# Optimization experiments

Measured on AMD Instinct MI355X. Metric: run time of the kernel, lower is better.

The kernel has to match this reference:

```python
import jax, jax.numpy as jnp
import numpy as np

B_SZ, L, H, P, G, N, CS = 2, 2048, 32, 64, 1, 128, 256


def _i8(k, shape):
    return jax.random.randint(k, shape, -127, 128, dtype=jnp.int32).astype(jnp.int8)


def setup_inputs() -> dict:
    key = jax.random.key(0)
    k = jax.random.split(key, 7)
    return {
        "x": _i8(k[0], (B_SZ, L, H, P)),          # quantized int8 activations
        "dt": _i8(k[1], (B_SZ, L, H)),
        "B": _i8(k[2], (B_SZ, L, G, N)),
        "C": _i8(k[3], (B_SZ, L, G, N)),
        "q_A_log": _i8(k[4], (H,)),               # int8 quantized A_log
        "q_D": _i8(k[5], (H,)),                   # int8 quantized D (D_has_hdim=False)
        "dt_bias": jax.random.normal(k[6], (H,), jnp.float32) * 0.1,
        "A_log_scale": jnp.float32(0.02),
        "D_scale": jnp.float32(0.01),
        "dt_scale": jnp.float32(0.03),
        "x_scale": jnp.float32(0.05),
        "B_scale": jnp.float32(0.05),
        "C_scale": jnp.float32(0.05),
    }


def _chunk_scan(x, dt, B, C, q_A_log, q_D, dt_bias,
                A_log_scale, D_scale, dt_scale, x_scale, B_scale, C_scale):
    f32 = jnp.float32
    b, l, h, p = x.shape
    g, n = B.shape[2], B.shape[3]
    cs = CS
    nc = l // cs

    # --- inline dequantization (per-tensor scales, nhead/ndim groups == 0) ---
    xf = x.astype(f32) * x_scale                       # (b, l, h, p)
    dtf = jax.nn.softplus(dt.astype(f32) * dt_scale + dt_bias)   # (b, l, h), dt_limit=(0, inf)
    A = -jnp.exp(q_A_log.astype(f32) * A_log_scale)    # (h,)
    Bf = B.astype(f32) * B_scale                       # (b, l, g, n)
    Cf = C.astype(f32) * C_scale

    # --- chunk the sequence ---
    xc = xf.reshape(b, nc, cs, h, p)
    dtc = dtf.reshape(b, nc, cs, h)
    Bc = Bf.reshape(b, nc, cs, g, n)
    Cc = Cf.reshape(b, nc, cs, g, n)
    rep = h // g
    Bh = jnp.repeat(Bc, rep, axis=3)                   # (b, nc, cs, h, n)
    Ch = jnp.repeat(Cc, rep, axis=3)

    dA = dtc * A                                       # (b, nc, cs, h), <= 0
    cum = jnp.cumsum(dA, axis=2)                       # cumulative log-decay within chunk

    # --- per-chunk states: sum_s exp(cum[-1]-cum[s]) * dt[s] * B[s] (x) x[s] ---
    decay_states = jnp.exp(cum[:, :, -1:, :] - cum)    # (b, nc, cs, h)
    states = jnp.einsum('bzlhn,bzlh,bzlhp->bzhpn', Bh, dtc * decay_states, xc)

    # --- inter-chunk recurrence (sequential scan over chunks) ---
    chunk_decay = jnp.exp(cum[:, :, -1, :])            # (b, nc, h)

    def step(carry, inp):
        s_c, d_c = inp                                 # (b, h, p, n), (b, h)
        new = d_c[:, :, None, None] * carry + s_c
        return new, carry                              # emit state entering this chunk

    states_t = jnp.moveaxis(states, 1, 0)              # (nc, b, h, p, n)
    decay_t = jnp.moveaxis(chunk_decay, 1, 0)          # (nc, b, h)
    final_state, prev_states = jax.lax.scan(
        step, jnp.zeros((b, h, p, n), f32), (states_t, decay_t))
    prev_states = jnp.moveaxis(prev_states, 0, 1)      # (b, nc, h, p, n)

    # --- inter-chunk output: C[l] . state_in * exp(cum[l]) ---
    y_inter = jnp.einsum('bzlhn,bzhpn,bzlh->bzlhp', Ch, prev_states, jnp.exp(cum))

    # --- intra-chunk output: causal (C.B) attention with decay weights ---
    cumT = jnp.moveaxis(cum, 3, 2)                     # (b, nc, h, cs)
    diff = cumT[..., :, None] - cumT[..., None, :]     # (b, nc, h, cs, cs): cum[l]-cum[s]
    mask = jnp.tril(jnp.ones((cs, cs), bool))
    decay_m = jnp.exp(jnp.where(mask, diff, -jnp.inf)) # zero above diagonal, no overflow
    scores = (jnp.einsum('bzlhn,bzshn->bzhls', Ch, Bh)
              * decay_m
              * jnp.moveaxis(dtc, 3, 2)[..., None, :])
    y_intra = jnp.einsum('bzhls,bzshp->bzlhp', scores, xc)

    # --- skip connection D * x (per-head D) ---
    Df = q_D.astype(f32) * D_scale                     # (h,)
    y = (y_intra + y_inter).reshape(b, l, h, p) + xf * Df[None, None, :, None]
    return y


def reference(x, dt, B, C, q_A_log, q_D, dt_bias,
              A_log_scale, D_scale, dt_scale, x_scale, B_scale, C_scale):
    return _chunk_scan(x, dt, B, C, q_A_log, q_D, dt_bias,
                       A_log_scale, D_scale, dt_scale, x_scale, B_scale, C_scale)
```

## Files before the change

### kernel.cpp

```cpp
#include <hip/hip_runtime.h>
#include <math.h>

#define BB 2
#define LSEQ 2048
#define H 32
#define PDIM 64
#define NDIM 128
#define CS 256
#define NC 8

typedef _Float16 half8 __attribute__((ext_vector_type(8)));
typedef _Float16 half4 __attribute__((ext_vector_type(4)));
typedef float floatx4 __attribute__((ext_vector_type(4)));


__device__ __forceinline__ int dot4i8(int a, int b, int c) {
#if __has_builtin(__builtin_amdgcn_sdot4)
    return __builtin_amdgcn_sdot4(a, b, c, false);
#else
    c += ((a << 24) >> 24) * ((b << 24) >> 24);
    c += ((a << 16) >> 24) * ((b << 16) >> 24);
    c += ((a << 8) >> 24) * ((b << 8) >> 24);
    c += (a >> 24) * (b >> 24);
    return c;
#endif
}

__global__ __launch_bounds__(256) void kA(
    const int* __restrict__ Bm, const int* __restrict__ Cm,
    const float* __restrict__ Bs_p, const float* __restrict__ Cs_p,
    float* __restrict__ CBt, _Float16* __restrict__ Bt16T, _Float16* __restrict__ C16T)
{
    __shared__ int Bi[64][33];
    __shared__ int Ci[64][33];
    int t = threadIdx.x;
    int r = blockIdx.x % 26;
    int zz = blockIdx.x / 26;
    int z = zz & 7, b = zz >> 3;
    int bz = b * NC + z;
    if (r < 10) {
        const int LT[10] = {0,1,1,2,2,2,3,3,3,3};
        const int ST[10] = {0,0,1,0,1,2,0,1,2,3};
        int l0 = LT[r] * 64, s0 = ST[r] * 64;
        const int* Bp = Bm + (size_t)(b * LSEQ + z * CS + s0) * NDIM;
        const int* Cp = Cm + (size_t)(b * LSEQ + z * CS + l0) * NDIM;
        for (int i = t; i < 64 * 32; i += 256) {
            int rr = i >> 5, k = i & 31;
            const int* sb = Bp + rr * NDIM + k * 4;
            const int* sc = Cp + rr * NDIM + k * 4;
            Bi[rr][k] = (sb[0] & 255) | ((sb[1] & 255) << 8) | ((sb[2] & 255) << 16) | ((sb[3] & 255) << 24);
            Ci[rr][k] = (sc[0] & 255) | ((sc[1] & 255) << 8) | ((sc[2] & 255) << 16) | ((sc[3] & 255) << 24);
        }
        __syncthreads();
        float cbscale = (*Bs_p) * (*Cs_p);
        int ll = t & 63, lg = t >> 6;
        int acc[16];
#pragma unroll
        for (int i = 0; i < 16; ++i) acc[i] = 0;
        for (int k = 0; k < 32; ++k) {
            int cw = Ci[ll][k];
#pragma unroll
            for (int si = 0; si < 16; ++si)
                acc[si] = dot4i8(cw, Bi[lg * 16 + si][k], acc[si]);
        }
        int l = l0 + ll;
        int l16 = l >> 4, lm = l & 15;
        int sb8 = (s0 + lg * 16) >> 3;
        float* bp = CBt + ((size_t)(bz * 16 + l16) * 32 + sb8) * 128 + lm * 8;
#pragma unroll
        for (int g = 0; g < 2; ++g) {
            floatx4 v0, v1;
#pragma unroll
            for (int i = 0; i < 4; ++i) {
                v0[i] = (float)acc[g * 8 + i] * cbscale;
                v1[i] = (float)acc[g * 8 + 4 + i] * cbscale;
            }
            *(floatx4*)(bp + g * 128) = v0;
            *(floatx4*)(bp + g * 128 + 4) = v1;
        }
    } else {
        int slice = r - 10;
        {
            int lm = t >> 4, n8 = t & 15;
            const int* cp = Cm + (size_t)(b * LSEQ + z * CS + slice * 16 + lm) * NDIM + n8 * 8;
            int4 c0 = *(const int4*)cp;
            int4 c1 = *(const int4*)(cp + 4);
            half8 v;
            v[0] = (_Float16)(float)c0.x; v[1] = (_Float16)(float)c0.y;
            v[2] = (_Float16)(float)c0.z; v[3] = (_Float16)(float)c0.w;
            v[4] = (_Float16)(float)c1.x; v[5] = (_Float16)(float)c1.y;
            v[6] = (_Float16)(float)c1.z; v[7] = (_Float16)(float)c1.w;
            *(half8*)(C16T + ((size_t)(bz * 16 + slice) * 16 + n8) * 128 + lm * 8) = v;
        }
        {
            int nm = t & 15, s8l = t >> 4;
            int n16 = slice & 7, s8 = (slice >> 3) * 16 + s8l;
            const int* bp = Bm + (size_t)(b * LSEQ + z * CS + s8 * 8) * NDIM + n16 * 16 + nm;
            half8 v;
#pragma unroll
            for (int j = 0; j < 8; ++j) v[j] = (_Float16)(float)bp[(size_t)j * NDIM];
            *(half8*)(Bt16T + ((size_t)(bz * 8 + n16) * 32 + s8) * 128 + nm * 8) = v;
        }
    }
}

#define XC_PITCH 132
__global__ __launch_bounds__(256) void k013(
    const int* __restrict__ dt, const int* __restrict__ qA, const float* __restrict__ dt_bias,
    const float* __restrict__ A_scale_p, const float* __restrict__ dt_scale_p,
    const int* __restrict__ xq, const float* __restrict__ xs_p, const float* __restrict__ Bs_p,
    const _Float16* __restrict__ Bt16T,
    float* __restrict__ cum, float* __restrict__ cdecay,
    _Float16* __restrict__ xTdtT, signed char* __restrict__ x8,
    float* __restrict__ states)
{
    __shared__ float cumS[CS];
    __shared__ float cA[CS], cB[CS];
    __shared__ float wsum[4];
    __shared__ _Float16 xcS[4 * 32 * XC_PITCH];
    int t = threadIdx.x;
    int h = blockIdx.x & 31, z = (blockIdx.x >> 5) & 7, b = blockIdx.x >> 8;
    int bz = b * NC + z, bzh = bz * H + h;
    int lane6 = t & 63, w = t >> 6;

    float A = -__expf((float)qA[h] * (*A_scale_p));
    float raw = (float)dt[(size_t)(b * LSEQ + z * CS + t) * H + h];
    float xin = raw * (*dt_scale_p) + dt_bias[h];
    float sp = (xin > 20.f) ? xin : log1pf(__expf(xin));
    float v = sp * A;
#pragma unroll
    for (int off = 1; off < 64; off <<= 1) {
        float u = __shfl_up(v, off, 64);
        if (lane6 >= off) v += u;
    }
    if (lane6 == 63) wsum[w] = v;
    __syncthreads();
    float add = 0.f;
    for (int wv = 0; wv < w; ++wv) add += wsum[wv];
    float cumv = v + add;
    float cl = wsum[0] + wsum[1] + wsum[2] + wsum[3];
    float xs = *xs_p;
    cum[bzh * CS + t] = cumv;
    if (t == 0) cdecay[bzh] = __expf(cl);
    cumS[t] = cumv;
    cA[t] = sp * xs;
    cB[t] = sp * __expf(cl - cumv) * xs * (*Bs_p);
    __syncthreads();

    int s8 = t & 31, pg = t >> 5;
    const int* xb = xq + ((size_t)(b * LSEQ + z * CS) * H + h) * PDIM + pg * 8;
    {
        half8 va[8], vc[8];
        signed char pk[8][8];
#pragma unroll
        for (int j = 0; j < 8; ++j) {
            int s = s8 * 8 + j;
            const int* xp = xb + (size_t)s * (H * PDIM);
            int4 lo = *(const int4*)xp;
            int4 hi = *(const int4*)(xp + 4);
            float a = cA[s], c = cB[s];
#define CVT(PL, V) { float xv = (float)(V); va[PL][j] = (_Float16)(xv * a); vc[PL][j] = (_Float16)(xv * c); pk[j][PL] = (signed char)(V); }
            CVT(0, lo.x) CVT(1, lo.y) CVT(2, lo.z) CVT(3, lo.w)
            CVT(4, hi.x) CVT(5, hi.y) CVT(6, hi.z) CVT(7, hi.w)
#undef CVT
        }
        int p16 = pg >> 1;
#pragma unroll
        for (int pl = 0; pl < 8; ++pl) {
            int p = pg * 8 + pl;
            *(half8*)(xTdtT + ((size_t)(bzh * 4 + p16) * 32 + s8) * 128 + (p & 15) * 8) = va[pl];
            xcS[(p16 * 32 + s8) * XC_PITCH + (p & 15) * 8 + 0] = vc[pl][0];
        }
#pragma unroll
        for (int pl = 0; pl < 8; ++pl) {
            int p = pg * 8 + pl;
            *(half8*)(xcS + (p16 * 32 + s8) * XC_PITCH + (p & 15) * 8) = vc[pl];
        }
        signed char* x8b = x8 + ((size_t)(b * LSEQ + z * CS) * H + h) * PDIM + pg * 8;
#pragma unroll
        for (int j = 0; j < 8; ++j)
            *(int2*)(x8b + (size_t)(s8 * 8 + j) * (H * PDIM)) = *(int2*)pk[j];
    }
    __syncthreads();

    int m = lane6 & 15, q = lane6 >> 4;
    const _Float16* bbase = Bt16T + (size_t)(bz * 8) * 32 * 128 + m * 8;
    const _Float16* abase = xcS + (w * 32) * XC_PITCH + m * 8;
    floatx4 acc[8] = {};
    for (int kk = 0; kk < 8; ++kk) {
        if (cl - cumS[kk * 32 + 31] < -30.f) continue;
        int s8k = kk * 4 + q;
        half8 a = *(const half8*)(abase + s8k * XC_PITCH);
#pragma unroll
        for (int nt = 0; nt < 8; ++nt) {
            half8 bf = *(const half8*)(bbase + ((size_t)nt * 32 + s8k) * 128);
            acc[nt] = __builtin_amdgcn_mfma_f32_16x16x32_f16(a, bf, acc[nt], 0, 0, 0);
        }
    }
    float* sb = states + (size_t)bzh * (PDIM * NDIM);
#pragma unroll
    for (int nt = 0; nt < 8; ++nt)
#pragma unroll
        for (int rr = 0; rr < 4; ++rr)
            sb[(size_t)(w * 16 + q * 4 + rr) * NDIM + nt * 16 + m] = acc[nt][rr];
}

__global__ __launch_bounds__(256) void k4_scan(
    const float* __restrict__ cdecay, const float* __restrict__ states,
    _Float16* __restrict__ statesHT)
{
    int idx = blockIdx.x * 256 + threadIdx.x;
    int n4 = (idx & 31) * 4, p = (idx >> 5) & 63, h = (idx >> 11) & 31, b = idx >> 16;
    int soff = p * 128 + n4;
    int toff = ((p >> 4) * 16 + (n4 >> 3)) * 128 + (p & 15) * 8 + (n4 & 7);
    floatx4 carry = {};
    for (int z = 0; z < NC; ++z) {
        int bzh = (b * NC + z) * H + h;
        floatx4 v = *(const floatx4*)(states + (size_t)bzh * 8192 + soff);
        float d = cdecay[bzh];
        half4 o;
#pragma unroll
        for (int i = 0; i < 4; ++i) o[i] = (_Float16)(carry[i] * 0.0625f);
        *(half4*)(statesHT + (size_t)bzh * 8192 + toff) = o;
#pragma unroll
        for (int i = 0; i < 4; ++i) carry[i] = d * carry[i] + v[i];
    }
}

__global__ __launch_bounds__(256) void k56(
    const signed char* __restrict__ x8, const int* __restrict__ qD,
    const float* __restrict__ cum, const float* __restrict__ CBt,
    const _Float16* __restrict__ xTdtT, const _Float16* __restrict__ C16T,
    const _Float16* __restrict__ statesHT,
    const float* __restrict__ Cs_p, const float* __restrict__ xs_p, const float* __restrict__ Ds_p,
    float* __restrict__ out)
{
    __shared__ float cumL[CS];
    __shared__ float ep[128][65];
    int t = threadIdx.x;
    int h = blockIdx.x & 31, z = (blockIdx.x >> 5) & 7, b = blockIdx.x >> 8;
    int bz = b * NC + z, bzh = bz * H + h;
    cumL[t] = cum[bzh * CS + t];
    __syncthreads();
    int w = t >> 6, lane = t & 63, m = lane & 15, q = lane >> 4;
    floatx4 acc[4][4] = {};

    const _Float16* shb = statesHT + (size_t)bzh * 8192 + m * 8;
    const _Float16* cbase = C16T + (size_t)bz * 16 * 16 * 128 + m * 8;
    bool interact[4];
#pragma unroll
    for (int j = 0; j < 4; ++j) interact[j] = (cumL[(4 * j + w) * 16] > -80.f);
    for (int kk = 0; kk < 4; ++kk) {
        int n8 = kk * 4 + q;
        half8 bf[4];
#pragma unroll
        for (int pt = 0; pt < 4; ++pt)
            bf[pt] = *(const half8*)(shb + (pt * 16 + n8) * 128);
#pragma unroll
        for (int j = 0; j < 4; ++j) {
            if (!interact[j]) continue;
            half8 ha = *(const half8*)(cbase + ((size_t)(4 * j + w) * 16 + n8) * 128);
#pragma unroll
            for (int pt = 0; pt < 4; ++pt)
                acc[j][pt] = __builtin_amdgcn_mfma_f32_16x16x32_f16(ha, bf[pt], acc[j][pt], 0, 0, 0);
        }
    }
    float Cs16 = (*Cs_p) * 16.0f;
#pragma unroll
    for (int j = 0; j < 4; ++j)
#pragma unroll
        for (int r = 0; r < 4; ++r) {
            float e = __expf(cumL[(4 * j + w) * 16 + q * 4 + r]) * Cs16;
#pragma unroll
            for (int pt = 0; pt < 4; ++pt) acc[j][pt][r] *= e;
        }

    const float* cbtb = CBt + (size_t)bz * 16 * 32 * 128 + m * 8;
    const _Float16* xb = xTdtT + (size_t)bzh * 4 * 32 * 128 + m * 8;
    for (int kk = 0; kk < 8; ++kk) {
        int jmin = (2 * kk - w + 3) >> 2;
        if (jmin < 0) jmin = 0;
        if (jmin > 3) continue;
        int s8 = kk * 4 + q;
        half8 bf[4];
#pragma unroll
        for (int pt = 0; pt < 4; ++pt)
            bf[pt] = *(const half8*)(xb + ((size_t)pt * 32 + s8) * 128);
        float cs_hi = cumL[kk * 32 + 31];
#pragma unroll
        for (int j = 0; j < 4; ++j) {
            if (j < jmin) continue;
            int l16 = 4 * j + w;
            if (cumL[l16 * 16] - cs_hi < -30.f) continue;
            int lA = l16 * 16 + m;
            float cum_l = cumL[lA];
            const float* cp = cbtb + ((size_t)l16 * 32 + s8) * 128;
            floatx4 c0 = *(const floatx4*)cp;
            floatx4 c1 = *(const floatx4*)(cp + 4);
            half8 a;
#pragma unroll
            for (int jj = 0; jj < 8; ++jj) {
                int s = kk * 32 + q * 8 + jj;
                float cb = (jj < 4) ? c0[jj] : c1[jj - 4];
                float wv = cb * __expf(cum_l - cumL[s]);
                a[jj] = (_Float16)((s <= lA) ? wv : 0.f);
            }
#pragma unroll
            for (int pt = 0; pt < 4; ++pt)
                acc[j][pt] = __builtin_amdgcn_mfma_f32_16x16x32_f16(a, bf[pt], acc[j][pt], 0, 0, 0);
        }
    }

    float xsDf = (*xs_p) * ((float)qD[h] * (*Ds_p));
    __syncthreads();
#pragma unroll
    for (int pass = 0; pass < 2; ++pass) {
#pragma unroll
        for (int jj = 0; jj < 2; ++jj) {
            int j = pass * 2 + jj;
            int lbase = (((4 * j + w) * 16) & 127) + q * 4;
#pragma unroll
            for (int r = 0; r < 4; ++r)
#pragma unroll
                for (int pt = 0; pt < 4; ++pt)
                    ep[lbase + r][pt * 16 + m] = acc[j][pt][r];
        }
        __syncthreads();
        int lloc = t >> 1;
        int l = pass * 128 + lloc;
        size_t go = ((size_t)(b * LSEQ + z * CS + l) * H + h) * PDIM + (t & 1) * 32;
        const float* er = &ep[lloc][(t & 1) * 32];
        const signed char* xp8 = x8 + go;
#pragma unroll
        for (int it = 0; it < 8; ++it) {
            int xw = *(const int*)(xp8 + it * 4);
            floatx4 v;
            v[0] = er[it * 4 + 0] + (float)((xw << 24) >> 24) * xsDf;
            v[1] = er[it * 4 + 1] + (float)((xw << 16) >> 24) * xsDf;
            v[2] = er[it * 4 + 2] + (float)((xw << 8) >> 24) * xsDf;
            v[3] = er[it * 4 + 3] + (float)(xw >> 24) * xsDf;
            *(floatx4*)(out + go + it * 4) = v;
        }
        __syncthreads();
    }
}

extern "C" void kernel_launch(void* const* d_in, const int* in_sizes, int n_in,
                              void* d_out, int out_size, void* d_ws, size_t ws_size,
                              hipStream_t stream)
{
    const int* xq = (const int*)d_in[0];
    const int* dt = (const int*)d_in[1];
    const int* Bm = (const int*)d_in[2];
    const int* Cm = (const int*)d_in[3];
    const int* qA = (const int*)d_in[4];
    const int* qD = (const int*)d_in[5];
    const float* dt_bias = (const float*)d_in[6];
    const float* A_scale = (const float*)d_in[7];
    const float* D_scale = (const float*)d_in[8];
    const float* dt_scale = (const float*)d_in[9];
    const float* x_scale = (const float*)d_in[10];
    const float* B_scale = (const float*)d_in[11];
    const float* C_scale = (const float*)d_in[12];
    float* out = (float*)d_out;

    char* ws = (char*)d_ws;
    float* cum          = (float*)(ws);
    float* cdecay       = (float*)(ws + 524288);
    float* CBt          = (float*)(ws + 526336);
    float* states       = (float*)(ws + 4720640);
    _Float16* xTdtT     = (_Float16*)(ws + 21497856);
    _Float16* statesHT  = (_Float16*)(ws + 38275072);
    _Float16* Bt16T     = (_Float16*)(ws + 46663680);
    _Float16* C16T      = (_Float16*)(ws + 47712256);
    signed char* x8     = (signed char*)(ws + 48760832);

    kA<<<dim3(416), dim3(256), 0, stream>>>(Bm, Cm, B_scale, C_scale, CBt, Bt16T, C16T);
    k013<<<dim3(512), dim3(256), 0, stream>>>(dt, qA, dt_bias, A_scale, dt_scale,
                                              xq, x_scale, B_scale, Bt16T,
                                              cum, cdecay, xTdtT, x8, states);
    k4_scan<<<dim3(512), dim3(256), 0, stream>>>(cdecay, states, statesHT);
    k56<<<dim3(512), dim3(256), 0, stream>>>(x8, qD, cum, CBt, xTdtT, C16T, statesHT,
                                             C_scale, x_scale, D_scale, out);
}
```

Before: 163.5 us.

## Split k013 and k56 work across twice as many blocks with balanced row pairing

New measurement: 169.3 us. +3.5%, slower.

```diff
diff --git a/kernel.cpp b/kernel.cpp
--- a/kernel.cpp
+++ b/kernel.cpp
@@ -117,9 +117,10 @@
     __shared__ float cumS[CS];
     __shared__ float cA[CS], cB[CS];
     __shared__ float wsum[4];
-    __shared__ _Float16 xcS[4 * 32 * XC_PITCH];
+    __shared__ _Float16 xcS[2 * 32 * XC_PITCH];
     int t = threadIdx.x;
-    int h = blockIdx.x & 31, z = (blockIdx.x >> 5) & 7, b = blockIdx.x >> 8;
+    int half = blockIdx.x & 1;
+    int h = (blockIdx.x >> 1) & 31, z = (blockIdx.x >> 6) & 7, b = blockIdx.x >> 9;
     int bz = b * NC + z, bzh = bz * H + h;
     int lane6 = t & 63, w = t >> 6;
 
@@ -140,69 +141,64 @@
     float cumv = v + add;
     float cl = wsum[0] + wsum[1] + wsum[2] + wsum[3];
     float xs = *xs_p;
-    cum[bzh * CS + t] = cumv;
-    if (t == 0) cdecay[bzh] = __expf(cl);
+    if (half == 0) {
+        cum[bzh * CS + t] = cumv;
+        if (t == 0) cdecay[bzh] = __expf(cl);
+    }
     cumS[t] = cumv;
     cA[t] = sp * xs;
     cB[t] = sp * __expf(cl - cumv) * xs * (*Bs_p);
     __syncthreads();
 
-    int s8 = t & 31, pg = t >> 5;
-    const int* xb = xq + ((size_t)(b * LSEQ + z * CS) * H + h) * PDIM + pg * 8;
+    int s8 = t & 31, pq = t >> 5;
+    const int* xb = xq + ((size_t)(b * LSEQ + z * CS) * H + h) * PDIM + half * 32 + pq * 4;
+    signed char* x8b = x8 + ((size_t)(b * LSEQ + z * CS) * H + h) * PDIM + half * 32 + pq * 4;
     {
-        half8 va[8], vc[8];
-        signed char pk[8][8];
+        half8 va[4], vc[4];
 #pragma unroll
         for (int j = 0; j < 8; ++j) {
             int s = s8 * 8 + j;
-            const int* xp = xb + (size_t)s * (H * PDIM);
-            int4 lo = *(const int4*)xp;
-            int4 hi = *(const int4*)(xp + 4);
+            int4 w4 = *(const int4*)(xb + (size_t)s * (H * PDIM));
             float a = cA[s], c = cB[s];
-#define CVT(PL, V) { float xv = (float)(V); va[PL][j] = (_Float16)(xv * a); vc[PL][j] = (_Float16)(xv * c); pk[j][PL] = (signed char)(V); }
-            CVT(0, lo.x) CVT(1, lo.y) CVT(2, lo.z) CVT(3, lo.w)
-            CVT(4, hi.x) CVT(5, hi.y) CVT(6, hi.z) CVT(7, hi.w)
+            signed char pk[4];
+#define CVT(PL, V) { float xv = (float)(V); va[PL][j] = (_Float16)(xv * a); vc[PL][j] = (_Float16)(xv * c); pk[PL] = (signed char)(V); }
+            CVT(0, w4.x) CVT(1, w4.y) CVT(2, w4.z) CVT(3, w4.w)
 #undef CVT
-        }
-        int p16 = pg >> 1;
-#pragma unroll
-        for (int pl = 0; pl < 8; ++pl) {
-            int p = pg * 8 + pl;
-            *(half8*)(xTdtT + ((size_t)(bzh * 4 + p16) * 32 + s8) * 128 + (p & 15) * 8) = va[pl];
-            xcS[(p16 * 32 + s8) * XC_PITCH + (p & 15) * 8 + 0] = vc[pl][0];
-        }
-#pragma unroll
-        for (int pl = 0; pl < 8; ++pl) {
-            int p = pg * 8 + pl;
-            *(half8*)(xcS + (p16 * 32 + s8) * XC_PITCH + (p & 15) * 8) = vc[pl];
-        }
-        signed char* x8b = x8 + ((size_t)(b * LSEQ + z * CS) * H + h) * PDIM + pg * 8;
-#pragma unroll
-        for (int j = 0; j < 8; ++j)
-            *(int2*)(x8b + (size_t)(s8 * 8 + j) * (H * PDIM)) = *(int2*)pk[j];
+            *(int*)pk;
+            *(int*)(x8b + (size_t)s * (H * PDIM)) = *(int*)pk;
+        }
+#pragma unroll
+        for (int pl = 0; pl < 4; ++pl) {
+            int ploc = pq * 4 + pl;
+            int p16l = ploc >> 4, pm = ploc & 15;
+            *(half8*)(xTdtT + ((size_t)(bzh * 4 + half * 2 + p16l) * 32 + s8) * 128 + pm * 8) = va[pl];
+            *(half8*)(xcS + (p16l * 32 + s8) * XC_PITCH + pm * 8) = vc[pl];
+        }
     }
     __syncthreads();
 
     int m = lane6 & 15, q = lane6 >> 4;
-    const _Float16* bbase = Bt16T + (size_t)(bz * 8) * 32 * 128 + m * 8;
-    const _Float16* abase = xcS + (w * 32) * XC_PITCH + m * 8;
-    floatx4 acc[8] = {};
+    int p16l = w & 1, ntb = (w >> 1) * 4;
+    const _Float16* abase = xcS + (p16l * 32) * XC_PITCH + m * 8;
+    const _Float16* bbase = Bt16T + ((size_t)(bz * 8 + ntb) * 32) * 128 + m * 8;
+    floatx4 acc[4] = {};
     for (int kk = 0; kk < 8; ++kk) {
         if (cl - cumS[kk * 32 + 31] < -30.f) continue;
         int s8k = kk * 4 + q;
         half8 a = *(const half8*)(abase + s8k * XC_PITCH);
 #pragma unroll
-        for (int nt = 0; nt < 8; ++nt) {
-            half8 bf = *(const half8*)(bbase + ((size_t)nt * 32 + s8k) * 128);
-            acc[nt] = __builtin_amdgcn_mfma_f32_16x16x32_f16(a, bf, acc[nt], 0, 0, 0);
-        }
-    }
+        for (int i = 0; i < 4; ++i) {
+            half8 bf = *(const half8*)(bbase + ((size_t)i * 32 + s8k) * 128);
+            acc[i] = __builtin_amdgcn_mfma_f32_16x16x32_f16(a, bf, acc[i], 0, 0, 0);
+        }
+    }
+    int p16 = half * 2 + p16l;
     float* sb = states + (size_t)bzh * (PDIM * NDIM);
 #pragma unroll
-    for (int nt = 0; nt < 8; ++nt)
+    for (int i = 0; i < 4; ++i)
 #pragma unroll
         for (int rr = 0; rr < 4; ++rr)
-            sb[(size_t)(w * 16 + q * 4 + rr) * NDIM + nt * 16 + m] = acc[nt][rr];
+            sb[(size_t)(p16 * 16 + q * 4 + rr) * NDIM + (ntb + i) * 16 + m] = acc[i][rr];
 }
 
 __global__ __launch_bounds__(256) void k4_scan(
@@ -238,18 +234,20 @@
     __shared__ float cumL[CS];
     __shared__ float ep[128][65];
     int t = threadIdx.x;
-    int h = blockIdx.x & 31, z = (blockIdx.x >> 5) & 7, b = blockIdx.x >> 8;
+    int parity = blockIdx.x & 1;
+    int h = (blockIdx.x >> 1) & 31, z = (blockIdx.x >> 6) & 7, b = blockIdx.x >> 9;
     int bz = b * NC + z, bzh = bz * H + h;
     cumL[t] = cum[bzh * CS + t];
     __syncthreads();
     int w = t >> 6, lane = t & 63, m = lane & 15, q = lane >> 4;
-    floatx4 acc[4][4] = {};
+    int l16a[2] = {parity + 2 * w, parity + 2 * (7 - w)};
+    floatx4 acc[2][4] = {};
 
     const _Float16* shb = statesHT + (size_t)bzh * 8192 + m * 8;
     const _Float16* cbase = C16T + (size_t)bz * 16 * 16 * 128 + m * 8;
-    bool interact[4];
-#pragma unroll
-    for (int j = 0; j < 4; ++j) interact[j] = (cumL[(4 * j + w) * 16] > -80.f);
+    bool interact[2];
+#pragma unroll
+    for (int j = 0; j < 2; ++j) interact[j] = (cumL[l16a[j] * 16] > -80.f);
     for (int kk = 0; kk < 4; ++kk) {
         int n8 = kk * 4 + q;
         half8 bf[4];
@@ -257,9 +255,9 @@
         for (int pt = 0; pt < 4; ++pt)
             bf[pt] = *(const half8*)(shb + (pt * 16 + n8) * 128);
 #pragma unroll
-        for (int j = 0; j < 4; ++j) {
+        for (int j = 0; j < 2; ++j) {
             if (!interact[j]) continue;
-            half8 ha = *(const half8*)(cbase + ((size_t)(4 * j + w) * 16 + n8) * 128);
+            half8 ha = *(const half8*)(cbase + ((size_t)l16a[j] * 16 + n8) * 128);
 #pragma unroll
             for (int pt = 0; pt < 4; ++pt)
                 acc[j][pt] = __builtin_amdgcn_mfma_f32_16x16x32_f16(ha, bf[pt], acc[j][pt], 0, 0, 0);
@@ -267,10 +265,10 @@
     }
     float Cs16 = (*Cs_p) * 16.0f;
 #pragma unroll
-    for (int j = 0; j < 4; ++j)
+    for (int j = 0; j < 2; ++j)
 #pragma unroll
         for (int r = 0; r < 4; ++r) {
-            float e = __expf(cumL[(4 * j + w) * 16 + q * 4 + r]) * Cs16;
+            float e = __expf(cumL[l16a[j] * 16 + q * 4 + r]) * Cs16;
 #pragma unroll
             for (int pt = 0; pt < 4; ++pt) acc[j][pt][r] *= e;
         }
@@ -278,20 +276,20 @@
     const float* cbtb = CBt + (size_t)bz * 16 * 32 * 128 + m * 8;
     const _Float16* xb = xTdtT + (size_t)bzh * 4 * 32 * 128 + m * 8;
     for (int kk = 0; kk < 8; ++kk) {
-        int jmin = (2 * kk - w + 3) >> 2;
-        if (jmin < 0) jmin = 0;
-        if (jmin > 3) continue;
+        bool ex[2];
+#pragma unroll
+        for (int j = 0; j < 2; ++j)
+            ex[j] = (2 * kk <= l16a[j]) && (cumL[l16a[j] * 16] - cumL[kk * 32 + 31] >= -30.f);
+        if (!ex[0] && !ex[1]) continue;
         int s8 = kk * 4 + q;
         half8 bf[4];
 #pragma unroll
         for (int pt = 0; pt < 4; ++pt)
             bf[pt] = *(const half8*)(xb + ((size_t)pt * 32 + s8) * 128);
-        float cs_hi = cumL[kk * 32 + 31];
-#pragma unroll
-        for (int j = 0; j < 4; ++j) {
-            if (j < jmin) continue;
-            int l16 = 4 * j + w;
-            if (cumL[l16 * 16] - cs_hi < -30.f) continue;
+#pragma unroll
+        for (int j = 0; j < 2; ++j) {
+            if (!ex[j]) continue;
+            int l16 = l16a[j];
             int lA = l16 * 16 + m;
             float cum_l = cumL[lA];
             const float* cp = cbtb + ((size_t)l16 * 32 + s8) * 128;
@@ -314,34 +312,31 @@
     float xsDf = (*xs_p) * ((float)qD[h] * (*Ds_p));
     __syncthreads();
 #pragma unroll
-    for (int pass = 0; pass < 2; ++pass) {
-#pragma unroll
-        for (int jj = 0; jj < 2; ++jj) {
-            int j = pass * 2 + jj;
-            int lbase = (((4 * j + w) * 16) & 127) + q * 4;
-#pragma unroll
-            for (int r = 0; r < 4; ++r)
-#pragma unroll
-                for (int pt = 0; pt < 4; ++pt)
-                    ep[lbase + r][pt * 16 + m] = acc[j][pt][r];
-        }
-        __syncthreads();
-        int lloc = t >> 1;
-        int l = pass * 128 + lloc;
-        size_t go = ((size_t)(b * LSEQ + z * CS + l) * H + h) * PDIM + (t & 1) * 32;
-        const float* er = &ep[lloc][(t & 1) * 32];
-        const signed char* xp8 = x8 + go;
-#pragma unroll
-        for (int it = 0; it < 8; ++it) {
-            int xw = *(const int*)(xp8 + it * 4);
-            floatx4 v;
-            v[0] = er[it * 4 + 0] + (float)((xw << 24) >> 24) * xsDf;
-            v[1] = er[it * 4 + 1] + (float)((xw << 16) >> 24) * xsDf;
-            v[2] = er[it * 4 + 2] + (float)((xw << 8) >> 24) * xsDf;
-            v[3] = er[it * 4 + 3] + (float)(xw >> 24) * xsDf;
-            *(floatx4*)(out + go + it * 4) = v;
-        }
-        __syncthreads();
+    for (int j = 0; j < 2; ++j) {
+        int kidx = (j == 0) ? w : 7 - w;
+        int lbase = kidx * 16 + q * 4;
+#pragma unroll
+        for (int r = 0; r < 4; ++r)
+#pragma unroll
+            for (int pt = 0; pt < 4; ++pt)
+                ep[lbase + r][pt * 16 + m] = acc[j][pt][r];
+    }
+    __syncthreads();
+    int lloc = t >> 1;
+    int kidx = lloc >> 4, row = lloc & 15;
+    int l = (parity + 2 * kidx) * 16 + row;
+    size_t go = ((size_t)(b * LSEQ + z * CS + l) * H + h) * PDIM + (t & 1) * 32;
+    const float* er = &ep[lloc][(t & 1) * 32];
+    const signed char* xp8 = x8 + go;
+#pragma unroll
+    for (int it = 0; it < 8; ++it) {
+        int xw = *(const int*)(xp8 + it * 4);
+        floatx4 vv;
+        vv[0] = er[it * 4 + 0] + (float)((xw << 24) >> 24) * xsDf;
+        vv[1] = er[it * 4 + 1] + (float)((xw << 16) >> 24) * xsDf;
+        vv[2] = er[it * 4 + 2] + (float)((xw << 8) >> 24) * xsDf;
+        vv[3] = er[it * 4 + 3] + (float)(xw >> 24) * xsDf;
+        *(floatx4*)(out + go + it * 4) = vv;
     }
 }
 
@@ -376,10 +371,10 @@
     signed char* x8     = (signed char*)(ws + 48760832);
 
     kA<<<dim3(416), dim3(256), 0, stream>>>(Bm, Cm, B_scale, C_scale, CBt, Bt16T, C16T);
-    k013<<<dim3(512), dim3(256), 0, stream>>>(dt, qA, dt_bias, A_scale, dt_scale,
-                                              xq, x_scale, B_scale, Bt16T,
-                                              cum, cdecay, xTdtT, x8, states);
+    k013<<<dim3(1024), dim3(256), 0, stream>>>(dt, qA, dt_bias, A_scale, dt_scale,
+                                               xq, x_scale, B_scale, Bt16T,
+                                               cum, cdecay, xTdtT, x8, states);
     k4_scan<<<dim3(512), dim3(256), 0, stream>>>(cdecay, states, statesHT);
-    k56<<<dim3(512), dim3(256), 0, stream>>>(x8, qD, cum, CBt, xTdtT, C16T, statesHT,
-                                             C_scale, x_scale, D_scale, out);
-}
+    k56<<<dim3(1024), dim3(256), 0, stream>>>(x8, qD, cum, CBt, xTdtT, C16T, statesHT,
+                                              C_scale, x_scale, D_scale, out);
+}
```

## Fuse chunk-state compute with inter-chunk scan and rebuild x*dt in output kernel

Applied to the files above, without the earlier changes.

Result: slower. 232.6 us (+42.2%).

```diff
diff --git a/kernel.cpp b/kernel.cpp
--- a/kernel.cpp
+++ b/kernel.cpp
@@ -10,7 +10,6 @@
 #define NC 8
 
 typedef _Float16 half8 __attribute__((ext_vector_type(8)));
-typedef _Float16 half4 __attribute__((ext_vector_type(4)));
 typedef float floatx4 __attribute__((ext_vector_type(4)));
 
 
@@ -29,7 +28,7 @@
 __global__ __launch_bounds__(256) void kA(
     const int* __restrict__ Bm, const int* __restrict__ Cm,
     const float* __restrict__ Bs_p, const float* __restrict__ Cs_p,
-    float* __restrict__ CBt, _Float16* __restrict__ Bt16T, _Float16* __restrict__ C16T)
+    _Float16* __restrict__ CBh, _Float16* __restrict__ Bt16T, _Float16* __restrict__ C16T)
 {
     __shared__ int Bi[64][33];
     __shared__ int Ci[64][33];
@@ -66,17 +65,13 @@
         int l = l0 + ll;
         int l16 = l >> 4, lm = l & 15;
         int sb8 = (s0 + lg * 16) >> 3;
-        float* bp = CBt + ((size_t)(bz * 16 + l16) * 32 + sb8) * 128 + lm * 8;
+        _Float16* bp = CBh + ((size_t)(bz * 16 + l16) * 32 + sb8) * 128 + lm * 8;
 #pragma unroll
         for (int g = 0; g < 2; ++g) {
-            floatx4 v0, v1;
-#pragma unroll
-            for (int i = 0; i < 4; ++i) {
-                v0[i] = (float)acc[g * 8 + i] * cbscale;
-                v1[i] = (float)acc[g * 8 + 4 + i] * cbscale;
-            }
-            *(floatx4*)(bp + g * 128) = v0;
-            *(floatx4*)(bp + g * 128 + 4) = v1;
+            half8 v;
+#pragma unroll
+            for (int i = 0; i < 8; ++i) v[i] = (_Float16)((float)acc[g * 8 + i] * cbscale);
+            *(half8*)(bp + g * 128) = v;
         }
     } else {
         int slice = r - 10;
@@ -104,144 +99,139 @@
     }
 }
 
-#define XC_PITCH 132
-__global__ __launch_bounds__(256) void k013(
+#define XCB_PITCH 264
+__global__ __launch_bounds__(256) void kB(
     const int* __restrict__ dt, const int* __restrict__ qA, const float* __restrict__ dt_bias,
     const float* __restrict__ A_scale_p, const float* __restrict__ dt_scale_p,
     const int* __restrict__ xq, const float* __restrict__ xs_p, const float* __restrict__ Bs_p,
     const _Float16* __restrict__ Bt16T,
-    float* __restrict__ cum, float* __restrict__ cdecay,
-    _Float16* __restrict__ xTdtT, signed char* __restrict__ x8,
-    float* __restrict__ states)
+    float* __restrict__ cum, float* __restrict__ cA,
+    signed char* __restrict__ x8, _Float16* __restrict__ statesHT)
 {
-    __shared__ float cumS[CS];
-    __shared__ float cA[CS], cB[CS];
+    __shared__ _Float16 xcS[16 * XCB_PITCH];
     __shared__ float wsum[4];
-    __shared__ _Float16 xcS[4 * 32 * XC_PITCH];
+    __shared__ float cumS8[8];
     int t = threadIdx.x;
-    int h = blockIdx.x & 31, z = (blockIdx.x >> 5) & 7, b = blockIdx.x >> 8;
-    int bz = b * NC + z, bzh = bz * H + h;
+    int h = blockIdx.x & 31, b = (blockIdx.x >> 5) & 1;
+    int pq = (blockIdx.x >> 6) & 3, nh = blockIdx.x >> 8;
     int lane6 = t & 63, w = t >> 6;
-
+    int m = lane6 & 15, q = lane6 >> 4;
+    int ntg = nh * 4 + w;
     float A = -__expf((float)qA[h] * (*A_scale_p));
-    float raw = (float)dt[(size_t)(b * LSEQ + z * CS + t) * H + h];
-    float xin = raw * (*dt_scale_p) + dt_bias[h];
-    float sp = (xin > 20.f) ? xin : log1pf(__expf(xin));
-    float v = sp * A;
-#pragma unroll
-    for (int off = 1; off < 64; off <<= 1) {
-        float u = __shfl_up(v, off, 64);
-        if (lane6 >= off) v += u;
-    }
-    if (lane6 == 63) wsum[w] = v;
-    __syncthreads();
-    float add = 0.f;
-    for (int wv = 0; wv < w; ++wv) add += wsum[wv];
-    float cumv = v + add;
-    float cl = wsum[0] + wsum[1] + wsum[2] + wsum[3];
-    float xs = *xs_p;
-    cum[bzh * CS + t] = cumv;
-    if (t == 0) cdecay[bzh] = __expf(cl);
-    cumS[t] = cumv;
-    cA[t] = sp * xs;
-    cB[t] = sp * __expf(cl - cumv) * xs * (*Bs_p);
-    __syncthreads();
-
-    int s8 = t & 31, pg = t >> 5;
-    const int* xb = xq + ((size_t)(b * LSEQ + z * CS) * H + h) * PDIM + pg * 8;
-    {
-        half8 va[8], vc[8];
-        signed char pk[8][8];
-#pragma unroll
-        for (int j = 0; j < 8; ++j) {
-            int s = s8 * 8 + j;
-            const int* xp = xb + (size_t)s * (H * PDIM);
-            int4 lo = *(const int4*)xp;
-            int4 hi = *(const int4*)(xp + 4);
-            float a = cA[s], c = cB[s];
-#define CVT(PL, V) { float xv = (float)(V); va[PL][j] = (_Float16)(xv * a); vc[PL][j] = (_Float16)(xv * c); pk[j][PL] = (signed char)(V); }
-            CVT(0, lo.x) CVT(1, lo.y) CVT(2, lo.z) CVT(3, lo.w)
-            CVT(4, hi.x) CVT(5, hi.y) CVT(6, hi.z) CVT(7, hi.w)
-#undef CVT
-        }
-        int p16 = pg >> 1;
-#pragma unroll
-        for (int pl = 0; pl < 8; ++pl) {
-            int p = pg * 8 + pl;
-            *(half8*)(xTdtT + ((size_t)(bzh * 4 + p16) * 32 + s8) * 128 + (p & 15) * 8) = va[pl];
-            xcS[(p16 * 32 + s8) * XC_PITCH + (p & 15) * 8 + 0] = vc[pl][0];
-        }
-#pragma unroll
-        for (int pl = 0; pl < 8; ++pl) {
-            int p = pg * 8 + pl;
-            *(half8*)(xcS + (p16 * 32 + s8) * XC_PITCH + (p & 15) * 8) = vc[pl];
-        }
-        signed char* x8b = x8 + ((size_t)(b * LSEQ + z * CS) * H + h) * PDIM + pg * 8;
-#pragma unroll
-        for (int j = 0; j < 8; ++j)
-            *(int2*)(x8b + (size_t)(s8 * 8 + j) * (H * PDIM)) = *(int2*)pk[j];
-    }
-    __syncthreads();
-
-    int m = lane6 & 15, q = lane6 >> 4;
-    const _Float16* bbase = Bt16T + (size_t)(bz * 8) * 32 * 128 + m * 8;
-    const _Float16* abase = xcS + (w * 32) * XC_PITCH + m * 8;
-    floatx4 acc[8] = {};
-    for (int kk = 0; kk < 8; ++kk) {
-        if (cl - cumS[kk * 32 + 31] < -30.f) continue;
-        int s8k = kk * 4 + q;
-        half8 a = *(const half8*)(abase + s8k * XC_PITCH);
-#pragma unroll
-        for (int nt = 0; nt < 8; ++nt) {
-            half8 bf = *(const half8*)(bbase + ((size_t)nt * 32 + s8k) * 128);
-            acc[nt] = __builtin_amdgcn_mfma_f32_16x16x32_f16(a, bf, acc[nt], 0, 0, 0);
-        }
-    }
-    float* sb = states + (size_t)bzh * (PDIM * NDIM);
-#pragma unroll
-    for (int nt = 0; nt < 8; ++nt)
-#pragma unroll
-        for (int rr = 0; rr < 4; ++rr)
-            sb[(size_t)(w * 16 + q * 4 + rr) * NDIM + nt * 16 + m] = acc[nt][rr];
-}
-
-__global__ __launch_bounds__(256) void k4_scan(
-    const float* __restrict__ cdecay, const float* __restrict__ states,
-    _Float16* __restrict__ statesHT)
-{
-    int idx = blockIdx.x * 256 + threadIdx.x;
-    int n4 = (idx & 31) * 4, p = (idx >> 5) & 63, h = (idx >> 11) & 31, b = idx >> 16;
-    int soff = p * 128 + n4;
-    int toff = ((p >> 4) * 16 + (n4 >> 3)) * 128 + (p & 15) * 8 + (n4 & 7);
-    floatx4 carry = {};
+    float dts = *dt_scale_p, bias = dt_bias[h];
+    float xs = *xs_p, Bs = *Bs_p;
+    bool wr_meta = (pq == 0 && nh == 0);
+    bool wr_x8 = (nh == 0);
+    float carry[4] = {0.f, 0.f, 0.f, 0.f};
+
+    float rawv = (float)dt[(size_t)(b * LSEQ + t) * H + h];
+    const int* xp0 = xq + ((size_t)(b * LSEQ + t) * H + h) * PDIM + pq * 16;
+    int4 xw0 = *(const int4*)xp0, xw1 = *(const int4*)(xp0 + 4);
+    int4 xw2 = *(const int4*)(xp0 + 8), xw3 = *(const int4*)(xp0 + 12);
+
     for (int z = 0; z < NC; ++z) {
-        int bzh = (b * NC + z) * H + h;
-        floatx4 v = *(const floatx4*)(states + (size_t)bzh * 8192 + soff);
-        float d = cdecay[bzh];
-        half4 o;
-#pragma unroll
-        for (int i = 0; i < 4; ++i) o[i] = (_Float16)(carry[i] * 0.0625f);
-        *(half4*)(statesHT + (size_t)bzh * 8192 + toff) = o;
-#pragma unroll
-        for (int i = 0; i < 4; ++i) carry[i] = d * carry[i] + v[i];
-    }
-}
-
-__global__ __launch_bounds__(256) void k56(
+        int bz = b * NC + z, bzh = bz * H + h;
+        __syncthreads();
+        float xin = rawv * dts + bias;
+        float sp = (xin > 20.f) ? xin : log1pf(__expf(xin));
+        float v = sp * A;
+#pragma unroll
+        for (int off = 1; off < 64; off <<= 1) {
+            float u = __shfl_up(v, off, 64);
+            if (lane6 >= off) v += u;
+        }
+        if (lane6 == 63) wsum[w] = v;
+        __syncthreads();
+        float add = 0.f;
+        for (int wv = 0; wv < w; ++wv) add += wsum[wv];
+        float cumv = v + add;
+        float cl = wsum[0] + wsum[1] + wsum[2] + wsum[3];
+        if ((t & 31) == 31) cumS8[t >> 5] = cumv;
+        if (wr_meta) {
+            cum[(size_t)bzh * CS + t] = cumv;
+            cA[(size_t)bzh * CS + t] = sp * xs;
+        }
+        float cBv = sp * __expf(cl - cumv) * xs * Bs;
+        int xi[16] = {xw0.x, xw0.y, xw0.z, xw0.w, xw1.x, xw1.y, xw1.z, xw1.w,
+                      xw2.x, xw2.y, xw2.z, xw2.w, xw3.x, xw3.y, xw3.z, xw3.w};
+        signed char pk[16];
+#pragma unroll
+        for (int pl = 0; pl < 16; ++pl) {
+            xcS[pl * XCB_PITCH + t] = (_Float16)((float)xi[pl] * cBv);
+            pk[pl] = (signed char)xi[pl];
+        }
+        if (wr_x8)
+            *(int4*)(x8 + ((size_t)(b * LSEQ + z * CS + t) * H + h) * PDIM + pq * 16) = *(int4*)pk;
+        if (z + 1 < NC) {
+            rawv = (float)dt[(size_t)(b * LSEQ + (z + 1) * CS + t) * H + h];
+            const int* xp = xq + ((size_t)(b * LSEQ + (z + 1) * CS + t) * H + h) * PDIM + pq * 16;
+            xw0 = *(const int4*)xp; xw1 = *(const int4*)(xp + 4);
+            xw2 = *(const int4*)(xp + 8); xw3 = *(const int4*)(xp + 12);
+        }
+        __syncthreads();
+        floatx4 accz = {};
+        const _Float16* ab = xcS + m * XCB_PITCH;
+        const _Float16* bb = Bt16T + ((size_t)(bz * 8 + ntg) * 32) * 128 + m * 8;
+        for (int kk = 0; kk < 8; ++kk) {
+            if (cl - cumS8[kk] < -30.f) continue;
+            half8 a = *(const half8*)(ab + kk * 32 + q * 8);
+            half8 bf = *(const half8*)(bb + (size_t)(kk * 4 + q) * 128);
+            accz = __builtin_amdgcn_mfma_f32_16x16x32_f16(a, bf, accz, 0, 0, 0);
+        }
+        float dz = __expf(cl);
+        size_t sbase = (size_t)bzh * 8192 + (size_t)(pq * 16 + ntg * 2 + (m >> 3)) * 128 + (m & 7);
+#pragma unroll
+        for (int rr = 0; rr < 4; ++rr) {
+            statesHT[sbase + (q * 4 + rr) * 8] = (_Float16)(carry[rr] * 0.0625f);
+            carry[rr] = dz * carry[rr] + accz[rr];
+        }
+    }
+}
+
+#define XT_PITCH 136
+__global__ __launch_bounds__(256) void kC(
     const signed char* __restrict__ x8, const int* __restrict__ qD,
-    const float* __restrict__ cum, const float* __restrict__ CBt,
-    const _Float16* __restrict__ xTdtT, const _Float16* __restrict__ C16T,
+    const float* __restrict__ cum, const float* __restrict__ cA,
+    const _Float16* __restrict__ CBh, const _Float16* __restrict__ C16T,
     const _Float16* __restrict__ statesHT,
     const float* __restrict__ Cs_p, const float* __restrict__ xs_p, const float* __restrict__ Ds_p,
     float* __restrict__ out)
 {
     __shared__ float cumL[CS];
-    __shared__ float ep[128][65];
+    __shared__ __align__(16) char smem[4 * 32 * XT_PITCH * 2];
+    _Float16* xT = (_Float16*)smem;
+    float (*ep)[65] = (float(*)[65])smem;
     int t = threadIdx.x;
     int h = blockIdx.x & 31, z = (blockIdx.x >> 5) & 7, b = blockIdx.x >> 8;
     int bz = b * NC + z, bzh = bz * H + h;
-    cumL[t] = cum[bzh * CS + t];
+    cumL[t] = cum[(size_t)bzh * CS + t];
+    float cav = cA[(size_t)bzh * CS + t];
+
+    {
+        const signed char* xrow = x8 + ((size_t)(b * LSEQ + z * CS + t) * H + h) * PDIM;
+        int s8 = t >> 3, sj = t & 7;
+        int rw[4] = {((const int4*)xrow)->x, 0, 0, 0};
+        int4 r4 = *(const int4*)xrow;
+        int4 r5 = *(const int4*)(xrow + 16);
+        int4 r6 = *(const int4*)(xrow + 32);
+        int4 r7 = *(const int4*)(xrow + 48);
+        int words[16] = {r4.x, r4.y, r4.z, r4.w, r5.x, r5.y, r5.z, r5.w,
+                         r6.x, r6.y, r6.z, r6.w, r7.x, r7.y, r7.z, r7.w};
+        (void)rw;
+#pragma unroll
+        for (int wi = 0; wi < 16; ++wi) {
+            int wv = words[wi];
+#pragma unroll
+            for (int bi = 0; bi < 4; ++bi) {
+                int p = wi * 4 + bi;
+                int val = (wv << (24 - 8 * bi)) >> 24;
+                xT[((p >> 4) * 32 + s8) * XT_PITCH + (p & 15) * 8 + sj] =
+                    (_Float16)((float)val * cav);
+            }
+        }
+    }
     __syncthreads();
+
     int w = t >> 6, lane = t & 63, m = lane & 15, q = lane >> 4;
     floatx4 acc[4][4] = {};
 
@@ -275,8 +265,7 @@
             for (int pt = 0; pt < 4; ++pt) acc[j][pt][r] *= e;
         }
 
-    const float* cbtb = CBt + (size_t)bz * 16 * 32 * 128 + m * 8;
-    const _Float16* xb = xTdtT + (size_t)bzh * 4 * 32 * 128 + m * 8;
+    const _Float16* cbtb = CBh + (size_t)bz * 16 * 32 * 128 + m * 8;
     for (int kk = 0; kk < 8; ++kk) {
         int jmin = (2 * kk - w + 3) >> 2;
         if (jmin < 0) jmin = 0;
@@ -285,24 +274,19 @@
         half8 bf[4];
 #pragma unroll
         for (int pt = 0; pt < 4; ++pt)
-            bf[pt] = *(const half8*)(xb + ((size_t)pt * 32 + s8) * 128);
-        float cs_hi = cumL[kk * 32 + 31];
-#pragma unroll
-        for (int j = 0; j < 4; ++j) {
-            if (j < jmin) continue;
+            bf[pt] = *(const half8*)(xT + (size_t)(pt * 32 + s8) * XT_PITCH + m * 8);
+#pragma unroll
+        for (int j = jmin; j < 4; ++j) {
             int l16 = 4 * j + w;
-            if (cumL[l16 * 16] - cs_hi < -30.f) continue;
+            if (cumL[l16 * 16] - cumL[kk * 32 + 31] < -30.f) continue;
             int lA = l16 * 16 + m;
             float cum_l = cumL[lA];
-            const float* cp = cbtb + ((size_t)l16 * 32 + s8) * 128;
-            floatx4 c0 = *(const floatx4*)cp;
-            floatx4 c1 = *(const floatx4*)(cp + 4);
+            half8 cb8 = *(const half8*)(cbtb + ((size_t)l16 * 32 + s8) * 128);
             half8 a;
 #pragma unroll
             for (int jj = 0; jj < 8; ++jj) {
                 int s = kk * 32 + q * 8 + jj;
-                float cb = (jj < 4) ? c0[jj] : c1[jj - 4];
-                float wv = cb * __expf(cum_l - cumL[s]);
+                float wv = (float)cb8[jj] * __expf(cum_l - cumL[s]);
                 a[jj] = (_Float16)((s <= lA) ? wv : 0.f);
             }
 #pragma unroll
@@ -334,12 +318,12 @@
 #pragma unroll
         for (int it = 0; it < 8; ++it) {
             int xw = *(const int*)(xp8 + it * 4);
-            floatx4 v;
-            v[0] = er[it * 4 + 0] + (float)((xw << 24) >> 24) * xsDf;
-            v[1] = er[it * 4 + 1] + (float)((xw << 16) >> 24) * xsDf;
-            v[2] = er[it * 4 + 2] + (float)((xw << 8) >> 24) * xsDf;
-            v[3] = er[it * 4 + 3] + (float)(xw >> 24) * xsDf;
-            *(floatx4*)(out + go + it * 4) = v;
+            floatx4 vv;
+            vv[0] = er[it * 4 + 0] + (float)((xw << 24) >> 24) * xsDf;
+            vv[1] = er[it * 4 + 1] + (float)((xw << 16) >> 24) * xsDf;
+            vv[2] = er[it * 4 + 2] + (float)((xw << 8) >> 24) * xsDf;
+            vv[3] = er[it * 4 + 3] + (float)(xw >> 24) * xsDf;
+            *(floatx4*)(out + go + it * 4) = vv;
         }
         __syncthreads();
     }
@@ -366,20 +350,17 @@
 
     char* ws = (char*)d_ws;
     float* cum          = (float*)(ws);
-    float* cdecay       = (float*)(ws + 524288);
-    float* CBt          = (float*)(ws + 526336);
-    float* states       = (float*)(ws + 4720640);
-    _Float16* xTdtT     = (_Float16*)(ws + 21497856);
-    _Float16* statesHT  = (_Float16*)(ws + 38275072);
-    _Float16* Bt16T     = (_Float16*)(ws + 46663680);
-    _Float16* C16T      = (_Float16*)(ws + 47712256);
-    signed char* x8     = (signed char*)(ws + 48760832);
-
-    kA<<<dim3(416), dim3(256), 0, stream>>>(Bm, Cm, B_scale, C_scale, CBt, Bt16T, C16T);
-    k013<<<dim3(512), dim3(256), 0, stream>>>(dt, qA, dt_bias, A_scale, dt_scale,
-                                              xq, x_scale, B_scale, Bt16T,
-                                              cum, cdecay, xTdtT, x8, states);
-    k4_scan<<<dim3(512), dim3(256), 0, stream>>>(cdecay, states, statesHT);
-    k56<<<dim3(512), dim3(256), 0, stream>>>(x8, qD, cum, CBt, xTdtT, C16T, statesHT,
-                                             C_scale, x_scale, D_scale, out);
-}
+    float* cA           = (float*)(ws + 524288);
+    _Float16* CBh       = (_Float16*)(ws + 1048576);
+    _Float16* statesHT  = (_Float16*)(ws + 3145728);
+    _Float16* Bt16T     = (_Float16*)(ws + 11534336);
+    _Float16* C16T      = (_Float16*)(ws + 12582912);
+    signed char* x8     = (signed char*)(ws + 13631488);
+
+    kA<<<dim3(416), dim3(256), 0, stream>>>(Bm, Cm, B_scale, C_scale, CBh, Bt16T, C16T);
+    kB<<<dim3(512), dim3(256), 0, stream>>>(dt, qA, dt_bias, A_scale, dt_scale,
+                                            xq, x_scale, B_scale, Bt16T,
+                                            cum, cA, x8, statesHT);
+    kC<<<dim3(512), dim3(256), 0, stream>>>(x8, qD, cum, cA, CBh, C16T, statesHT,
+                                            C_scale, x_scale, D_scale, out);
+}
```
